# Kernel optimization log

Hardware: AMD Instinct MI355X
Metric: run time of the kernel (lower is better)

Reference implementation:

```python
import jax, jax.numpy as jnp
import numpy as np

IN_PLANES = 768
RATIO = 16


def setup_inputs() -> dict:
    key = jax.random.key(0)
    k1, k2, k3 = jax.random.split(key, 3)
    x = jax.random.normal(k1, (32, IN_PLANES, 56, 56), dtype=jnp.float32)
    hidden = IN_PLANES // RATIO
    # Conv2d(C, C//r, 1, bias=False) weight -> [C//r, C]; Conv2d(C//r, C, 1) -> [C, C//r]
    w1 = jax.random.normal(k2, (hidden, IN_PLANES), dtype=jnp.float32) * (1.0 / np.sqrt(IN_PLANES))
    w2 = jax.random.normal(k3, (IN_PLANES, hidden), dtype=jnp.float32) * (1.0 / np.sqrt(hidden))
    return {"x": x, "w1": w1, "w2": w2}


def _mlp(v, w1, w2):
    # v: [B, C]; shared 1x1-conv MLP with exact GELU (torch default)
    h = jax.nn.gelu(jnp.einsum("bc,hc->bh", v, w1), approximate=False)
    return jnp.einsum("bh,ch->bc", h, w2)


def reference(x, w1, w2):
    # x: [B, C, H, W]
    avg = jnp.mean(x, axis=(2, 3))  # [B, C]
    mx = jnp.max(x, axis=(2, 3))    # [B, C]
    gate = jax.nn.sigmoid(_mlp(avg, w1, w2) + _mlp(mx, w1, w2))  # [B, C]
    return x * gate[:, :, None, None]
```

## Files before the change

### kernel.cpp

```cpp
#include <hip/hip_runtime.h>
#include <math.h>

#define BATCH 32
#define CH 768
#define HW 3136
#define HW4 (HW/4)
#define HID 48
#define PLANES (BATCH*CH)
#define WPB 4

typedef float nfloat4 __attribute__((ext_vector_type(4)));

__global__ __launch_bounds__(256) void cbam_pool(const float* __restrict__ x,
                                                 float* __restrict__ avg,
                                                 float* __restrict__ mx) {
    const int wave = threadIdx.x >> 6;
    const int lane = threadIdx.x & 63;
    const int plane = blockIdx.x * WPB + wave;
    const nfloat4* xp = reinterpret_cast<const nfloat4*>(x + (size_t)plane * HW);

    float s = 0.0f;
    float m = -INFINITY;
    #pragma unroll
    for (int j = 0; j < 3; ++j) {
        const int base = j * 256 + lane;
        nfloat4 a = xp[base];
        nfloat4 b = xp[base + 64];
        nfloat4 c = xp[base + 128];
        nfloat4 d = xp[base + 192];
        s += ((a.x + a.y) + (a.z + a.w)) + ((b.x + b.y) + (b.z + b.w))
           + ((c.x + c.y) + (c.z + c.w)) + ((d.x + d.y) + (d.z + d.w));
        float ma = fmaxf(fmaxf(a.x, a.y), fmaxf(a.z, a.w));
        float mb = fmaxf(fmaxf(b.x, b.y), fmaxf(b.z, b.w));
        float mc = fmaxf(fmaxf(c.x, c.y), fmaxf(c.z, c.w));
        float md = fmaxf(fmaxf(d.x, d.y), fmaxf(d.z, d.w));
        m = fmaxf(m, fmaxf(fmaxf(ma, mb), fmaxf(mc, md)));
    }
    if (lane < 16) {
        nfloat4 a = xp[768 + lane];
        s += (a.x + a.y) + (a.z + a.w);
        m = fmaxf(m, fmaxf(fmaxf(a.x, a.y), fmaxf(a.z, a.w)));
    }
    for (int off = 32; off > 0; off >>= 1) {
        s += __shfl_down(s, off, 64);
        m = fmaxf(m, __shfl_down(m, off, 64));
    }
    if (lane == 0) {
        avg[plane] = s * (1.0f / (float)HW);
        mx[plane]  = m;
    }
}

__global__ __launch_bounds__(256) void cbam_mlp(const float* __restrict__ avg,
                                                const float* __restrict__ mx,
                                                const float* __restrict__ w1,
                                                const float* __restrict__ w2,
                                                float* __restrict__ gate) {
    const int b = blockIdx.x;
    __shared__ float sa[CH];
    __shared__ float sv[CH];
    __shared__ float ha[HID];
    __shared__ float hm[HID];
    __shared__ float hsum[HID];

    for (int i = threadIdx.x; i < CH; i += 256) {
        sa[i] = avg[b * CH + i];
        sv[i] = mx[b * CH + i];
    }
    __syncthreads();

    if (threadIdx.x < 2 * HID) {
        const bool is_avg = threadIdx.x < HID;
        const int h = is_avg ? threadIdx.x : threadIdx.x - HID;
        const float4* in4 = reinterpret_cast<const float4*>(is_avg ? sa : sv);
        const float4* wr4 = reinterpret_cast<const float4*>(w1 + (size_t)h * CH);
        float acc = 0.0f;
        #pragma unroll 8
        for (int k = 0; k < CH / 4; ++k) {
            float4 a = in4[k];
            float4 w = wr4[k];
            acc += a.x * w.x + a.y * w.y + a.z * w.z + a.w * w.w;
        }
        float g = 0.5f * acc * (1.0f + erff(acc * 0.70710678118654752f));
        if (is_avg) ha[h] = g; else hm[h] = g;
    }
    __syncthreads();
    if (threadIdx.x < HID) hsum[threadIdx.x] = ha[threadIdx.x] + hm[threadIdx.x];
    __syncthreads();

    for (int c = threadIdx.x; c < CH; c += 256) {
        const float4* wr4 = reinterpret_cast<const float4*>(w2 + (size_t)c * HID);
        const float4* hs4 = reinterpret_cast<const float4*>(hsum);
        float acc = 0.0f;
        #pragma unroll
        for (int h = 0; h < HID / 4; ++h) {
            float4 a = hs4[h];
            float4 w = wr4[h];
            acc += a.x * w.x + a.y * w.y + a.z * w.z + a.w * w.w;
        }
        gate[b * CH + c] = 1.0f / (1.0f + expf(-acc));
    }
}

__global__ __launch_bounds__(256) void cbam_scale(const float* __restrict__ x,
                                                  const float* __restrict__ gate,
                                                  float* __restrict__ out) {
    const int wave = threadIdx.x >> 6;
    const int lane = threadIdx.x & 63;
    const int plane = (PLANES - 1) - (blockIdx.x * WPB + wave);
    const float g = gate[plane];
    const nfloat4* xp = reinterpret_cast<const nfloat4*>(x + (size_t)plane * HW);
    nfloat4* op = reinterpret_cast<nfloat4*>(out + (size_t)plane * HW);

    #pragma unroll
    for (int j = 0; j < 3; ++j) {
        const int base = j * 256 + lane;
        nfloat4 a = xp[base];
        nfloat4 b = xp[base + 64];
        nfloat4 c = xp[base + 128];
        nfloat4 d = xp[base + 192];
        a.x *= g; a.y *= g; a.z *= g; a.w *= g;
        b.x *= g; b.y *= g; b.z *= g; b.w *= g;
        c.x *= g; c.y *= g; c.z *= g; c.w *= g;
        d.x *= g; d.y *= g; d.z *= g; d.w *= g;
        __builtin_nontemporal_store(a, &op[base]);
        __builtin_nontemporal_store(b, &op[base + 64]);
        __builtin_nontemporal_store(c, &op[base + 128]);
        __builtin_nontemporal_store(d, &op[base + 192]);
    }
    if (lane < 16) {
        const int i = 768 + lane;
        nfloat4 a = xp[i];
        a.x *= g; a.y *= g; a.z *= g; a.w *= g;
        __builtin_nontemporal_store(a, &op[i]);
    }
}

extern "C" void kernel_launch(void* const* d_in, const int* in_sizes, int n_in,
                              void* d_out, int out_size, void* d_ws, size_t ws_size,
                              hipStream_t stream) {
    const float* x  = (const float*)d_in[0];
    const float* w1 = (const float*)d_in[1];
    const float* w2 = (const float*)d_in[2];
    float* out = (float*)d_out;

    float* avg  = (float*)d_ws;
    float* mx   = avg + PLANES;
    float* gate = mx + PLANES;

    cbam_pool<<<PLANES / WPB, 256, 0, stream>>>(x, avg, mx);
    cbam_mlp<<<BATCH, 256, 0, stream>>>(avg, mx, w1, w2, gate);
    cbam_scale<<<PLANES / WPB, 256, 0, stream>>>(x, gate, out);
}
```

Baseline: 170.1 us.

## Fuse pool, MLP and scale into one cooperative kernel with grid syncs

Replaces the three kernel launches with a single cooperative kernel of 256 blocks. Each wave pools 24 planes, a grid sync follows, 32 blocks compute the MLP gate, a second grid sync follows, and then each wave scales its planes in reverse order so recently read data may still be in cache. The aim is to remove launch gaps and gain some cache reuse of x between the pool and scale phases. In exchange it runs only 4 waves per CU for a bandwidth-bound stream, and most blocks sit idle through the serial MLP phase between the syncs. The old three-kernel path stays as a fallback if the cooperative launch fails.

```diff
diff --git a/kernel.cpp b/kernel.cpp
--- a/kernel.cpp
+++ b/kernel.cpp
@@ -1,5 +1,8 @@
 #include <hip/hip_runtime.h>
+#include <hip/hip_cooperative_groups.h>
 #include <math.h>
+
+namespace cg = cooperative_groups;
 
 #define BATCH 32
 #define CH 768
@@ -7,9 +10,142 @@
 #define HW4 (HW/4)
 #define HID 48
 #define PLANES (BATCH*CH)
+#define NBLK 256
+#define PPB (PLANES/NBLK)
+#define PPW (PPB/4)
 #define WPB 4
 
 typedef float nfloat4 __attribute__((ext_vector_type(4)));
+
+__global__ __launch_bounds__(256, 4) void cbam_fused(const float* __restrict__ x,
+                                                     const float* __restrict__ w1,
+                                                     const float* __restrict__ w2,
+                                                     float* __restrict__ out,
+                                                     float* __restrict__ avg,
+                                                     float* __restrict__ mx,
+                                                     float* __restrict__ gate) {
+    cg::grid_group grid = cg::this_grid();
+    const int wave = threadIdx.x >> 6;
+    const int lane = threadIdx.x & 63;
+
+    for (int pi = 0; pi < PPW; ++pi) {
+        const int plane = blockIdx.x * PPB + wave * PPW + pi;
+        const nfloat4* xp = reinterpret_cast<const nfloat4*>(x + (size_t)plane * HW);
+        float s = 0.0f;
+        float m = -INFINITY;
+        #pragma unroll
+        for (int j = 0; j < 3; ++j) {
+            const int base = j * 256 + lane;
+            nfloat4 a = xp[base];
+            nfloat4 b = xp[base + 64];
+            nfloat4 c = xp[base + 128];
+            nfloat4 d = xp[base + 192];
+            s += ((a.x + a.y) + (a.z + a.w)) + ((b.x + b.y) + (b.z + b.w))
+               + ((c.x + c.y) + (c.z + c.w)) + ((d.x + d.y) + (d.z + d.w));
+            float ma = fmaxf(fmaxf(a.x, a.y), fmaxf(a.z, a.w));
+            float mb = fmaxf(fmaxf(b.x, b.y), fmaxf(b.z, b.w));
+            float mc = fmaxf(fmaxf(c.x, c.y), fmaxf(c.z, c.w));
+            float md = fmaxf(fmaxf(d.x, d.y), fmaxf(d.z, d.w));
+            m = fmaxf(m, fmaxf(fmaxf(ma, mb), fmaxf(mc, md)));
+        }
+        if (lane < 16) {
+            nfloat4 a = xp[768 + lane];
+            s += (a.x + a.y) + (a.z + a.w);
+            m = fmaxf(m, fmaxf(fmaxf(a.x, a.y), fmaxf(a.z, a.w)));
+        }
+        for (int off = 32; off > 0; off >>= 1) {
+            s += __shfl_down(s, off, 64);
+            m = fmaxf(m, __shfl_down(m, off, 64));
+        }
+        if (lane == 0) {
+            avg[plane] = s * (1.0f / (float)HW);
+            mx[plane]  = m;
+        }
+    }
+
+    __threadfence();
+    grid.sync();
+
+    __shared__ float sa[CH];
+    __shared__ float sv[CH];
+    __shared__ float ha[HID];
+    __shared__ float hm[HID];
+    __shared__ float hsum[HID];
+
+    if (blockIdx.x < BATCH) {
+        const int b = blockIdx.x;
+
+        for (int i = threadIdx.x; i < CH; i += 256) {
+            sa[i] = avg[b * CH + i];
+            sv[i] = mx[b * CH + i];
+        }
+        __syncthreads();
+
+        if (threadIdx.x < 2 * HID) {
+            const bool is_avg = threadIdx.x < HID;
+            const int h = is_avg ? threadIdx.x : threadIdx.x - HID;
+            const float4* in4 = reinterpret_cast<const float4*>(is_avg ? sa : sv);
+            const float4* wr4 = reinterpret_cast<const float4*>(w1 + (size_t)h * CH);
+            float acc = 0.0f;
+            #pragma unroll 4
+            for (int k = 0; k < CH / 4; ++k) {
+                float4 a = in4[k];
+                float4 w = wr4[k];
+                acc += a.x * w.x + a.y * w.y + a.z * w.z + a.w * w.w;
+            }
+            float g = 0.5f * acc * (1.0f + erff(acc * 0.70710678118654752f));
+            if (is_avg) ha[h] = g; else hm[h] = g;
+        }
+        __syncthreads();
+        if (threadIdx.x < HID) hsum[threadIdx.x] = ha[threadIdx.x] + hm[threadIdx.x];
+        __syncthreads();
+
+        for (int c = threadIdx.x; c < CH; c += 256) {
+            const float4* wr4 = reinterpret_cast<const float4*>(w2 + (size_t)c * HID);
+            const float4* hs4 = reinterpret_cast<const float4*>(hsum);
+            float acc = 0.0f;
+            #pragma unroll
+            for (int h = 0; h < HID / 4; ++h) {
+                float4 a = hs4[h];
+                float4 w = wr4[h];
+                acc += a.x * w.x + a.y * w.y + a.z * w.z + a.w * w.w;
+            }
+            gate[b * CH + c] = 1.0f / (1.0f + expf(-acc));
+        }
+    }
+
+    __threadfence();
+    grid.sync();
+
+    for (int pi = PPW - 1; pi >= 0; --pi) {
+        const int plane = blockIdx.x * PPB + wave * PPW + pi;
+        const float g = gate[plane];
+        const nfloat4* xp = reinterpret_cast<const nfloat4*>(x + (size_t)plane * HW);
+        nfloat4* op = reinterpret_cast<nfloat4*>(out + (size_t)plane * HW);
+        #pragma unroll
+        for (int j = 0; j < 3; ++j) {
+            const int base = j * 256 + lane;
+            nfloat4 a = xp[base];
+            nfloat4 b = xp[base + 64];
+            nfloat4 c = xp[base + 128];
+            nfloat4 d = xp[base + 192];
+            a.x *= g; a.y *= g; a.z *= g; a.w *= g;
+            b.x *= g; b.y *= g; b.z *= g; b.w *= g;
+            c.x *= g; c.y *= g; c.z *= g; c.w *= g;
+            d.x *= g; d.y *= g; d.z *= g; d.w *= g;
+            __builtin_nontemporal_store(a, &op[base]);
+            __builtin_nontemporal_store(b, &op[base + 64]);
+            __builtin_nontemporal_store(c, &op[base + 128]);
+            __builtin_nontemporal_store(d, &op[base + 192]);
+        }
+        if (lane < 16) {
+            const int i = 768 + lane;
+            nfloat4 a = xp[i];
+            a.x *= g; a.y *= g; a.z *= g; a.w *= g;
+            __builtin_nontemporal_store(a, &op[i]);
+        }
+    }
+}
 
 __global__ __launch_bounds__(256) void cbam_pool(const float* __restrict__ x,
                                                  float* __restrict__ avg,
@@ -148,7 +284,13 @@
     float* mx   = avg + PLANES;
     float* gate = mx + PLANES;
 
-    cbam_pool<<<PLANES / WPB, 256, 0, stream>>>(x, avg, mx);
-    cbam_mlp<<<BATCH, 256, 0, stream>>>(avg, mx, w1, w2, gate);
-    cbam_scale<<<PLANES / WPB, 256, 0, stream>>>(x, gate, out);
-}
+    void* args[] = { (void*)&x, (void*)&w1, (void*)&w2, (void*)&out,
+                     (void*)&avg, (void*)&mx, (void*)&gate };
+    hipError_t err = hipLaunchCooperativeKernel((const void*)cbam_fused,
+                                                dim3(NBLK), dim3(256), args, 0, stream);
+    if (err != hipSuccess) {
+        cbam_pool<<<PLANES / WPB, 256, 0, stream>>>(x, avg, mx);
+        cbam_mlp<<<BATCH, 256, 0, stream>>>(avg, mx, w1, w2, gate);
+        cbam_scale<<<PLANES / WPB, 256, 0, stream>>>(x, gate, out);
+    }
+}
```

Measured after the change: 277.8 us. +63.3%, slower.

## Fuse pool, MLP and scale into one persistent kernel with per-image barrier

Applied to the files above, without the earlier changes.

Replaces the three kernels with one kernel of 1024 blocks. Each block pools 24 planes of one image, then waits on a per-image atomic counter until all 32 blocks for that image have finished. Each block then recomputes the hidden MLP layer and only the 24 gate values it needs before scaling its own planes. This removes two launches and the separate gate round-trip, and re-reads planes soon after pooling so more of x may still be in cache. In exchange it adds a memset, spin-wait barriers that rely on all blocks being co-resident, and 32 redundant copies of the first MLP layer per image.

```diff
diff --git a/kernel.cpp b/kernel.cpp
--- a/kernel.cpp
+++ b/kernel.cpp
@@ -7,65 +7,88 @@
 #define HW4 (HW/4)
 #define HID 48
 #define PLANES (BATCH*CH)
-#define WPB 4
+#define NBLK 1024
+#define BPI 32
+#define PPB 24
+#define PPW 6
+#define CNT_STRIDE 32
 
 typedef float nfloat4 __attribute__((ext_vector_type(4)));
 
-__global__ __launch_bounds__(256) void cbam_pool(const float* __restrict__ x,
-                                                 float* __restrict__ avg,
-                                                 float* __restrict__ mx) {
+__global__ __launch_bounds__(256, 4) void cbam_onepass(
+    const float* __restrict__ x,
+    const float* __restrict__ w1,
+    const float* __restrict__ w2,
+    float* __restrict__ out,
+    float* __restrict__ avg,
+    float* __restrict__ mx,
+    int* __restrict__ cnt)
+{
+    const int g    = blockIdx.x;
+    const int img  = g >> 5;
+    const int sub  = g & 31;
     const int wave = threadIdx.x >> 6;
     const int lane = threadIdx.x & 63;
-    const int plane = blockIdx.x * WPB + wave;
-    const nfloat4* xp = reinterpret_cast<const nfloat4*>(x + (size_t)plane * HW);
 
-    float s = 0.0f;
-    float m = -INFINITY;
-    #pragma unroll
-    for (int j = 0; j < 3; ++j) {
-        const int base = j * 256 + lane;
-        nfloat4 a = xp[base];
-        nfloat4 b = xp[base + 64];
-        nfloat4 c = xp[base + 128];
-        nfloat4 d = xp[base + 192];
-        s += ((a.x + a.y) + (a.z + a.w)) + ((b.x + b.y) + (b.z + b.w))
-           + ((c.x + c.y) + (c.z + c.w)) + ((d.x + d.y) + (d.z + d.w));
-        float ma = fmaxf(fmaxf(a.x, a.y), fmaxf(a.z, a.w));
-        float mb = fmaxf(fmaxf(b.x, b.y), fmaxf(b.z, b.w));
-        float mc = fmaxf(fmaxf(c.x, c.y), fmaxf(c.z, c.w));
-        float md = fmaxf(fmaxf(d.x, d.y), fmaxf(d.z, d.w));
-        m = fmaxf(m, fmaxf(fmaxf(ma, mb), fmaxf(mc, md)));
-    }
-    if (lane < 16) {
-        nfloat4 a = xp[768 + lane];
-        s += (a.x + a.y) + (a.z + a.w);
-        m = fmaxf(m, fmaxf(fmaxf(a.x, a.y), fmaxf(a.z, a.w)));
-    }
-    for (int off = 32; off > 0; off >>= 1) {
-        s += __shfl_down(s, off, 64);
-        m = fmaxf(m, __shfl_down(m, off, 64));
-    }
-    if (lane == 0) {
-        avg[plane] = s * (1.0f / (float)HW);
-        mx[plane]  = m;
-    }
-}
-
-__global__ __launch_bounds__(256) void cbam_mlp(const float* __restrict__ avg,
-                                                const float* __restrict__ mx,
-                                                const float* __restrict__ w1,
-                                                const float* __restrict__ w2,
-                                                float* __restrict__ gate) {
-    const int b = blockIdx.x;
     __shared__ float sa[CH];
     __shared__ float sv[CH];
     __shared__ float ha[HID];
     __shared__ float hm[HID];
     __shared__ float hsum[HID];
+    __shared__ float sgate[PPB];
+
+    for (int pi = 0; pi < PPW; ++pi) {
+        const int k = wave * PPW + pi;
+        const int plane = img * CH + sub + BPI * k;
+        const nfloat4* xp = reinterpret_cast<const nfloat4*>(x + (size_t)plane * HW);
+        float s = 0.0f;
+        float m = -INFINITY;
+        #pragma unroll
+        for (int j = 0; j < 3; ++j) {
+            const int base = j * 256 + lane;
+            nfloat4 a = xp[base];
+            nfloat4 b = xp[base + 64];
+            nfloat4 c = xp[base + 128];
+            nfloat4 d = xp[base + 192];
+            s += ((a.x + a.y) + (a.z + a.w)) + ((b.x + b.y) + (b.z + b.w))
+               + ((c.x + c.y) + (c.z + c.w)) + ((d.x + d.y) + (d.z + d.w));
+            float ma = fmaxf(fmaxf(a.x, a.y), fmaxf(a.z, a.w));
+            float mb = fmaxf(fmaxf(b.x, b.y), fmaxf(b.z, b.w));
+            float mc = fmaxf(fmaxf(c.x, c.y), fmaxf(c.z, c.w));
+            float md = fmaxf(fmaxf(d.x, d.y), fmaxf(d.z, d.w));
+            m = fmaxf(m, fmaxf(fmaxf(ma, mb), fmaxf(mc, md)));
+        }
+        if (lane < 16) {
+            nfloat4 a = xp[768 + lane];
+            s += (a.x + a.y) + (a.z + a.w);
+            m = fmaxf(m, fmaxf(fmaxf(a.x, a.y), fmaxf(a.z, a.w)));
+        }
+        for (int off = 32; off > 0; off >>= 1) {
+            s += __shfl_down(s, off, 64);
+            m = fmaxf(m, __shfl_down(m, off, 64));
+        }
+        if (lane == 0) {
+            avg[plane] = s * (1.0f / (float)HW);
+            mx[plane]  = m;
+        }
+    }
+
+    __threadfence();
+    __syncthreads();
+    if (threadIdx.x == 0) {
+        __hip_atomic_fetch_add(&cnt[img * CNT_STRIDE], 1,
+                               __ATOMIC_ACQ_REL, __HIP_MEMORY_SCOPE_AGENT);
+        while (__hip_atomic_load(&cnt[img * CNT_STRIDE],
+                                 __ATOMIC_ACQUIRE, __HIP_MEMORY_SCOPE_AGENT) < BPI) {
+            __builtin_amdgcn_s_sleep(8);
+        }
+    }
+    __syncthreads();
+    __threadfence();
 
     for (int i = threadIdx.x; i < CH; i += 256) {
-        sa[i] = avg[b * CH + i];
-        sv[i] = mx[b * CH + i];
+        sa[i] = avg[img * CH + i];
+        sv[i] = mx[img * CH + i];
     }
     __syncthreads();
 
@@ -76,19 +99,20 @@
         const float4* wr4 = reinterpret_cast<const float4*>(w1 + (size_t)h * CH);
         float acc = 0.0f;
         #pragma unroll 8
-        for (int k = 0; k < CH / 4; ++k) {
-            float4 a = in4[k];
-            float4 w = wr4[k];
+        for (int kk = 0; kk < CH / 4; ++kk) {
+            float4 a = in4[kk];
+            float4 w = wr4[kk];
             acc += a.x * w.x + a.y * w.y + a.z * w.z + a.w * w.w;
         }
-        float g = 0.5f * acc * (1.0f + erff(acc * 0.70710678118654752f));
-        if (is_avg) ha[h] = g; else hm[h] = g;
+        float gg = 0.5f * acc * (1.0f + erff(acc * 0.70710678118654752f));
+        if (is_avg) ha[h] = gg; else hm[h] = gg;
     }
     __syncthreads();
     if (threadIdx.x < HID) hsum[threadIdx.x] = ha[threadIdx.x] + hm[threadIdx.x];
     __syncthreads();
 
-    for (int c = threadIdx.x; c < CH; c += 256) {
+    if (threadIdx.x < PPB) {
+        const int c = sub + BPI * threadIdx.x;
         const float4* wr4 = reinterpret_cast<const float4*>(w2 + (size_t)c * HID);
         const float4* hs4 = reinterpret_cast<const float4*>(hsum);
         float acc = 0.0f;
@@ -98,41 +122,38 @@
             float4 w = wr4[h];
             acc += a.x * w.x + a.y * w.y + a.z * w.z + a.w * w.w;
         }
-        gate[b * CH + c] = 1.0f / (1.0f + expf(-acc));
+        sgate[threadIdx.x] = 1.0f / (1.0f + expf(-acc));
     }
-}
+    __syncthreads();
 
-__global__ __launch_bounds__(256) void cbam_scale(const float* __restrict__ x,
-                                                  const float* __restrict__ gate,
-                                                  float* __restrict__ out) {
-    const int wave = threadIdx.x >> 6;
-    const int lane = threadIdx.x & 63;
-    const int plane = (PLANES - 1) - (blockIdx.x * WPB + wave);
-    const float g = gate[plane];
-    const nfloat4* xp = reinterpret_cast<const nfloat4*>(x + (size_t)plane * HW);
-    nfloat4* op = reinterpret_cast<nfloat4*>(out + (size_t)plane * HW);
-
-    #pragma unroll
-    for (int j = 0; j < 3; ++j) {
-        const int base = j * 256 + lane;
-        nfloat4 a = xp[base];
-        nfloat4 b = xp[base + 64];
-        nfloat4 c = xp[base + 128];
-        nfloat4 d = xp[base + 192];
-        a.x *= g; a.y *= g; a.z *= g; a.w *= g;
-        b.x *= g; b.y *= g; b.z *= g; b.w *= g;
-        c.x *= g; c.y *= g; c.z *= g; c.w *= g;
-        d.x *= g; d.y *= g; d.z *= g; d.w *= g;
-        __builtin_nontemporal_store(a, &op[base]);
-        __builtin_nontemporal_store(b, &op[base + 64]);
-        __builtin_nontemporal_store(c, &op[base + 128]);
-        __builtin_nontemporal_store(d, &op[base + 192]);
-    }
-    if (lane < 16) {
-        const int i = 768 + lane;
-        nfloat4 a = xp[i];
-        a.x *= g; a.y *= g; a.z *= g; a.w *= g;
-        __builtin_nontemporal_store(a, &op[i]);
+    for (int pi = 0; pi < PPW; ++pi) {
+        const int k = wave * PPW + pi;
+        const int plane = img * CH + sub + BPI * k;
+        const float gfac = sgate[k];
+        const nfloat4* xp = reinterpret_cast<const nfloat4*>(x + (size_t)plane * HW);
+        nfloat4* op = reinterpret_cast<nfloat4*>(out + (size_t)plane * HW);
+        #pragma unroll
+        for (int j = 0; j < 3; ++j) {
+            const int base = j * 256 + lane;
+            nfloat4 a = xp[base];
+            nfloat4 b = xp[base + 64];
+            nfloat4 c = xp[base + 128];
+            nfloat4 d = xp[base + 192];
+            a.x *= gfac; a.y *= gfac; a.z *= gfac; a.w *= gfac;
+            b.x *= gfac; b.y *= gfac; b.z *= gfac; b.w *= gfac;
+            c.x *= gfac; c.y *= gfac; c.z *= gfac; c.w *= gfac;
+            d.x *= gfac; d.y *= gfac; d.z *= gfac; d.w *= gfac;
+            __builtin_nontemporal_store(a, &op[base]);
+            __builtin_nontemporal_store(b, &op[base + 64]);
+            __builtin_nontemporal_store(c, &op[base + 128]);
+            __builtin_nontemporal_store(d, &op[base + 192]);
+        }
+        if (lane < 16) {
+            const int i = 768 + lane;
+            nfloat4 a = xp[i];
+            a.x *= gfac; a.y *= gfac; a.z *= gfac; a.w *= gfac;
+            __builtin_nontemporal_store(a, &op[i]);
+        }
     }
 }
 
@@ -144,11 +165,11 @@
     const float* w2 = (const float*)d_in[2];
     float* out = (float*)d_out;
 
-    float* avg  = (float*)d_ws;
-    float* mx   = avg + PLANES;
-    float* gate = mx + PLANES;
+    float* avg = (float*)d_ws;
+    float* mx  = avg + PLANES;
+    int*   cnt = (int*)(mx + PLANES);
 
-    cbam_pool<<<PLANES / WPB, 256, 0, stream>>>(x, avg, mx);
-    cbam_mlp<<<BATCH, 256, 0, stream>>>(avg, mx, w1, w2, gate);
-    cbam_scale<<<PLANES / WPB, 256, 0, stream>>>(x, gate, out);
+    hipMemsetAsync(cnt, 0, BATCH * CNT_STRIDE * sizeof(int), stream);
+
+    cbam_onepass<<<NBLK, 256, 0, stream>>>(x, w1, w2, out, avg, mx, cnt);
 }
```

Result: slower. 496.8 us (+192.0%).

## Fuse pool, MLP and scale into one kernel with per-image atomic handoff

Applied to the files above, without the earlier changes.

Merges the pooling, MLP and scaling kernels into a single launch. Each block pools four planes and bumps a per-image counter. The last block to arrive for an image computes that image's gate and sets a release flag, while the other blocks spin on it and then scale their own planes. The aim is to re-read each plane of x soon after pooling it, so the second read is likely to hit L2 or Infinity Cache instead of HBM, and to drop two kernel launch boundaries. In exchange it adds a memset, atomic counters and spin-waiting blocks that hold CU slots, and it depends on blocks being dispatched roughly in order to avoid stalls or deadlock.

```diff
diff --git a/kernel.cpp b/kernel.cpp
--- a/kernel.cpp
+++ b/kernel.cpp
@@ -7,132 +7,165 @@
 #define HW4 (HW/4)
 #define HID 48
 #define PLANES (BATCH*CH)
-#define WPB 4
+#define BPI 192
+#define NBLK (BATCH*BPI)
+#define PAD 32
 
 typedef float nfloat4 __attribute__((ext_vector_type(4)));
 
-__global__ __launch_bounds__(256) void cbam_pool(const float* __restrict__ x,
-                                                 float* __restrict__ avg,
-                                                 float* __restrict__ mx) {
+__global__ __launch_bounds__(256, 8) void cbam_onekernel(
+    const float* __restrict__ x,
+    const float* __restrict__ w1,
+    const float* __restrict__ w2,
+    float* __restrict__ out,
+    float* __restrict__ avg,
+    float* __restrict__ mx,
+    float* __restrict__ gate,
+    int* __restrict__ cnt,
+    int* __restrict__ flag)
+{
+    const int g    = blockIdx.x;
+    const int img  = g / BPI;
+    const int sub  = g % BPI;
     const int wave = threadIdx.x >> 6;
     const int lane = threadIdx.x & 63;
-    const int plane = blockIdx.x * WPB + wave;
-    const nfloat4* xp = reinterpret_cast<const nfloat4*>(x + (size_t)plane * HW);
+    const int plane = img * CH + sub * 4 + wave;
 
-    float s = 0.0f;
-    float m = -INFINITY;
-    #pragma unroll
-    for (int j = 0; j < 3; ++j) {
-        const int base = j * 256 + lane;
-        nfloat4 a = xp[base];
-        nfloat4 b = xp[base + 64];
-        nfloat4 c = xp[base + 128];
-        nfloat4 d = xp[base + 192];
-        s += ((a.x + a.y) + (a.z + a.w)) + ((b.x + b.y) + (b.z + b.w))
-           + ((c.x + c.y) + (c.z + c.w)) + ((d.x + d.y) + (d.z + d.w));
-        float ma = fmaxf(fmaxf(a.x, a.y), fmaxf(a.z, a.w));
-        float mb = fmaxf(fmaxf(b.x, b.y), fmaxf(b.z, b.w));
-        float mc = fmaxf(fmaxf(c.x, c.y), fmaxf(c.z, c.w));
-        float md = fmaxf(fmaxf(d.x, d.y), fmaxf(d.z, d.w));
-        m = fmaxf(m, fmaxf(fmaxf(ma, mb), fmaxf(mc, md)));
-    }
-    if (lane < 16) {
-        nfloat4 a = xp[768 + lane];
-        s += (a.x + a.y) + (a.z + a.w);
-        m = fmaxf(m, fmaxf(fmaxf(a.x, a.y), fmaxf(a.z, a.w)));
-    }
-    for (int off = 32; off > 0; off >>= 1) {
-        s += __shfl_down(s, off, 64);
-        m = fmaxf(m, __shfl_down(m, off, 64));
-    }
-    if (lane == 0) {
-        avg[plane] = s * (1.0f / (float)HW);
-        mx[plane]  = m;
-    }
-}
-
-__global__ __launch_bounds__(256) void cbam_mlp(const float* __restrict__ avg,
-                                                const float* __restrict__ mx,
-                                                const float* __restrict__ w1,
-                                                const float* __restrict__ w2,
-                                                float* __restrict__ gate) {
-    const int b = blockIdx.x;
     __shared__ float sa[CH];
     __shared__ float sv[CH];
     __shared__ float ha[HID];
     __shared__ float hm[HID];
     __shared__ float hsum[HID];
+    __shared__ int   sIsLast;
 
-    for (int i = threadIdx.x; i < CH; i += 256) {
-        sa[i] = avg[b * CH + i];
-        sv[i] = mx[b * CH + i];
+    {
+        const nfloat4* xp = reinterpret_cast<const nfloat4*>(x + (size_t)plane * HW);
+        float s = 0.0f;
+        float m = -INFINITY;
+        #pragma unroll
+        for (int j = 0; j < 3; ++j) {
+            const int base = j * 256 + lane;
+            nfloat4 a = xp[base];
+            nfloat4 b = xp[base + 64];
+            nfloat4 c = xp[base + 128];
+            nfloat4 d = xp[base + 192];
+            s += ((a.x + a.y) + (a.z + a.w)) + ((b.x + b.y) + (b.z + b.w))
+               + ((c.x + c.y) + (c.z + c.w)) + ((d.x + d.y) + (d.z + d.w));
+            float ma = fmaxf(fmaxf(a.x, a.y), fmaxf(a.z, a.w));
+            float mb = fmaxf(fmaxf(b.x, b.y), fmaxf(b.z, b.w));
+            float mc = fmaxf(fmaxf(c.x, c.y), fmaxf(c.z, c.w));
+            float md = fmaxf(fmaxf(d.x, d.y), fmaxf(d.z, d.w));
+            m = fmaxf(m, fmaxf(fmaxf(ma, mb), fmaxf(mc, md)));
+        }
+        if (lane < 16) {
+            nfloat4 a = xp[768 + lane];
+            s += (a.x + a.y) + (a.z + a.w);
+            m = fmaxf(m, fmaxf(fmaxf(a.x, a.y), fmaxf(a.z, a.w)));
+        }
+        for (int off = 32; off > 0; off >>= 1) {
+            s += __shfl_down(s, off, 64);
+            m = fmaxf(m, __shfl_down(m, off, 64));
+        }
+        if (lane == 0) {
+            __hip_atomic_store(&avg[plane], s * (1.0f / (float)HW),
+                               __ATOMIC_RELAXED, __HIP_MEMORY_SCOPE_AGENT);
+            __hip_atomic_store(&mx[plane], m,
+                               __ATOMIC_RELAXED, __HIP_MEMORY_SCOPE_AGENT);
+        }
+    }
+
+    __syncthreads();
+    if (threadIdx.x == 0) {
+        int old = __hip_atomic_fetch_add(&cnt[img * PAD], 1,
+                                         __ATOMIC_ACQ_REL, __HIP_MEMORY_SCOPE_AGENT);
+        sIsLast = (old == BPI - 1);
     }
     __syncthreads();
 
-    if (threadIdx.x < 2 * HID) {
-        const bool is_avg = threadIdx.x < HID;
-        const int h = is_avg ? threadIdx.x : threadIdx.x - HID;
-        const float4* in4 = reinterpret_cast<const float4*>(is_avg ? sa : sv);
-        const float4* wr4 = reinterpret_cast<const float4*>(w1 + (size_t)h * CH);
-        float acc = 0.0f;
-        #pragma unroll 8
-        for (int k = 0; k < CH / 4; ++k) {
-            float4 a = in4[k];
-            float4 w = wr4[k];
-            acc += a.x * w.x + a.y * w.y + a.z * w.z + a.w * w.w;
+    if (sIsLast) {
+        for (int i = threadIdx.x; i < CH; i += 256) {
+            sa[i] = __hip_atomic_load(&avg[img * CH + i], __ATOMIC_RELAXED, __HIP_MEMORY_SCOPE_AGENT);
+            sv[i] = __hip_atomic_load(&mx[img * CH + i],  __ATOMIC_RELAXED, __HIP_MEMORY_SCOPE_AGENT);
         }
-        float g = 0.5f * acc * (1.0f + erff(acc * 0.70710678118654752f));
-        if (is_avg) ha[h] = g; else hm[h] = g;
+        __syncthreads();
+
+        if (threadIdx.x < 2 * HID) {
+            const bool is_avg = threadIdx.x < HID;
+            const int h = is_avg ? threadIdx.x : threadIdx.x - HID;
+            const float4* in4 = reinterpret_cast<const float4*>(is_avg ? sa : sv);
+            const float4* wr4 = reinterpret_cast<const float4*>(w1 + (size_t)h * CH);
+            float acc = 0.0f;
+            #pragma unroll 8
+            for (int k = 0; k < CH / 4; ++k) {
+                float4 a = in4[k];
+                float4 w = wr4[k];
+                acc += a.x * w.x + a.y * w.y + a.z * w.z + a.w * w.w;
+            }
+            float ge = 0.5f * acc * (1.0f + erff(acc * 0.70710678118654752f));
+            if (is_avg) ha[h] = ge; else hm[h] = ge;
+        }
+        __syncthreads();
+        if (threadIdx.x < HID) hsum[threadIdx.x] = ha[threadIdx.x] + hm[threadIdx.x];
+        __syncthreads();
+
+        for (int c = threadIdx.x; c < CH; c += 256) {
+            const float4* wr4 = reinterpret_cast<const float4*>(w2 + (size_t)c * HID);
+            const float4* hs4 = reinterpret_cast<const float4*>(hsum);
+            float acc = 0.0f;
+            #pragma unroll
+            for (int h = 0; h < HID / 4; ++h) {
+                float4 a = hs4[h];
+                float4 w = wr4[h];
+                acc += a.x * w.x + a.y * w.y + a.z * w.z + a.w * w.w;
+            }
+            __hip_atomic_store(&gate[img * CH + c], 1.0f / (1.0f + expf(-acc)),
+                               __ATOMIC_RELAXED, __HIP_MEMORY_SCOPE_AGENT);
+        }
+        __syncthreads();
+        if (threadIdx.x == 0) {
+            __hip_atomic_store(&flag[img * PAD], 1,
+                               __ATOMIC_RELEASE, __HIP_MEMORY_SCOPE_AGENT);
+        }
+    }
+
+    if (threadIdx.x == 0) {
+        while (__hip_atomic_load(&flag[img * PAD], __ATOMIC_RELAXED, __HIP_MEMORY_SCOPE_AGENT) == 0) {
+            __builtin_amdgcn_s_sleep(16);
+        }
+        (void)__hip_atomic_load(&flag[img * PAD], __ATOMIC_ACQUIRE, __HIP_MEMORY_SCOPE_AGENT);
     }
     __syncthreads();
-    if (threadIdx.x < HID) hsum[threadIdx.x] = ha[threadIdx.x] + hm[threadIdx.x];
-    __syncthreads();
 
-    for (int c = threadIdx.x; c < CH; c += 256) {
-        const float4* wr4 = reinterpret_cast<const float4*>(w2 + (size_t)c * HID);
-        const float4* hs4 = reinterpret_cast<const float4*>(hsum);
-        float acc = 0.0f;
+    {
+        float gv = 0.0f;
+        if (lane == 0)
+            gv = __hip_atomic_load(&gate[plane], __ATOMIC_RELAXED, __HIP_MEMORY_SCOPE_AGENT);
+        gv = __shfl(gv, 0, 64);
+
+        const nfloat4* xp = reinterpret_cast<const nfloat4*>(x + (size_t)plane * HW);
+        nfloat4* op = reinterpret_cast<nfloat4*>(out + (size_t)plane * HW);
         #pragma unroll
-        for (int h = 0; h < HID / 4; ++h) {
-            float4 a = hs4[h];
-            float4 w = wr4[h];
-            acc += a.x * w.x + a.y * w.y + a.z * w.z + a.w * w.w;
+        for (int j = 0; j < 3; ++j) {
+            const int base = j * 256 + lane;
+            nfloat4 a = xp[base];
+            nfloat4 b = xp[base + 64];
+            nfloat4 c = xp[base + 128];
+            nfloat4 d = xp[base + 192];
+            a.x *= gv; a.y *= gv; a.z *= gv; a.w *= gv;
+            b.x *= gv; b.y *= gv; b.z *= gv; b.w *= gv;
+            c.x *= gv; c.y *= gv; c.z *= gv; c.w *= gv;
+            d.x *= gv; d.y *= gv; d.z *= gv; d.w *= gv;
+            __builtin_nontemporal_store(a, &op[base]);
+            __builtin_nontemporal_store(b, &op[base + 64]);
+            __builtin_nontemporal_store(c, &op[base + 128]);
+            __builtin_nontemporal_store(d, &op[base + 192]);
         }
-        gate[b * CH + c] = 1.0f / (1.0f + expf(-acc));
-    }
-}
-
-__global__ __launch_bounds__(256) void cbam_scale(const float* __restrict__ x,
-                                                  const float* __restrict__ gate,
-                                                  float* __restrict__ out) {
-    const int wave = threadIdx.x >> 6;
-    const int lane = threadIdx.x & 63;
-    const int plane = (PLANES - 1) - (blockIdx.x * WPB + wave);
-    const float g = gate[plane];
-    const nfloat4* xp = reinterpret_cast<const nfloat4*>(x + (size_t)plane * HW);
-    nfloat4* op = reinterpret_cast<nfloat4*>(out + (size_t)plane * HW);
-
-    #pragma unroll
-    for (int j = 0; j < 3; ++j) {
-        const int base = j * 256 + lane;
-        nfloat4 a = xp[base];
-        nfloat4 b = xp[base + 64];
-        nfloat4 c = xp[base + 128];
-        nfloat4 d = xp[base + 192];
-        a.x *= g; a.y *= g; a.z *= g; a.w *= g;
-        b.x *= g; b.y *= g; b.z *= g; b.w *= g;
-        c.x *= g; c.y *= g; c.z *= g; c.w *= g;
-        d.x *= g; d.y *= g; d.z *= g; d.w *= g;
-        __builtin_nontemporal_store(a, &op[base]);
-        __builtin_nontemporal_store(b, &op[base + 64]);
-        __builtin_nontemporal_store(c, &op[base + 128]);
-        __builtin_nontemporal_store(d, &op[base + 192]);
-    }
-    if (lane < 16) {
-        const int i = 768 + lane;
-        nfloat4 a = xp[i];
-        a.x *= g; a.y *= g; a.z *= g; a.w *= g;
-        __builtin_nontemporal_store(a, &op[i]);
+        if (lane < 16) {
+            const int i = 768 + lane;
+            nfloat4 a = xp[i];
+            a.x *= gv; a.y *= gv; a.z *= gv; a.w *= gv;
+            __builtin_nontemporal_store(a, &op[i]);
+        }
     }
 }
 
@@ -147,8 +180,10 @@
     float* avg  = (float*)d_ws;
     float* mx   = avg + PLANES;
     float* gate = mx + PLANES;
+    int*   cnt  = (int*)(gate + PLANES);
+    int*   flag = cnt + BATCH * PAD;
 
-    cbam_pool<<<PLANES / WPB, 256, 0, stream>>>(x, avg, mx);
-    cbam_mlp<<<BATCH, 256, 0, stream>>>(avg, mx, w1, w2, gate);
-    cbam_scale<<<PLANES / WPB, 256, 0, stream>>>(x, gate, out);
+    hipMemsetAsync(cnt, 0, 2 * BATCH * PAD * sizeof(int), stream);
+
+    cbam_onekernel<<<NBLK, 256, 0, stream>>>(x, w1, w2, out, avg, mx, gate, cnt, flag);
 }
```

Result: slower. 548.2 us (+222.3%).
